# Kernel optimization log

Measured on AMD Instinct MI355X. Metric: run time of the kernel, lower is better.

## Reference

```python
import jax, jax.numpy as jnp
import numpy as np

B, D, I, H, K = 1024, 128, 64, 256, 8
HE = 2 * H  # encoder cell width (mu || log_sigma2)


def setup_inputs() -> dict:
    key = jax.random.key(0)
    ks = jax.random.split(key, 20)
    g = lambda i, shape, s=0.05: jax.random.normal(ks[i], shape, dtype=jnp.float32) * s
    return dict(
        X=g(0, (B, D, I), 1.0),
        W=jax.random.randint(ks[1], (B, D, I), 0, 2).astype(jnp.int32),
        noise=g(2, (B, H), 1.0),
        A=g(3, (D, I)),  # imputation template (learned)
        enc_Wx=g(4, (I, 4 * HE)), enc_Wh=g(5, (HE, 4 * HE)), enc_b=jnp.zeros((4 * HE,), jnp.float32),
        enc_pi=g(6, (HE,)), enc_pf=g(7, (HE,)), enc_po=g(8, (HE,)),
        dec_Wx=g(9, (I, 4 * H)), dec_Wh=g(10, (H, 4 * H)), dec_b=jnp.zeros((4 * H,), jnp.float32),
        dec_pi=g(11, (H,)), dec_pf=g(12, (H,)), dec_po=g(13, (H,)),
        out_w=g(14, (H, I)), out_b=jnp.full((I,), 0.1, jnp.float32),
        mu_c_unscaled=g(15, (K, H)), sigma2_c_unscaled=g(16, (K, H)), phi_c_unscaled=g(17, (K,)),
    )


def peephole_lstm(x_seq, Wx, Wh, b, pi, pf, po, h0, c0):
    """Keras PeepholeLSTMCell, gate order i,f,c,o. x_seq: [T,B,I] -> (hs [T,B,n], hT, cT)."""
    def step(carry, x):
        h, c = carry
        z = x @ Wx + h @ Wh + b
        zi, zf, zc, zo = jnp.split(z, 4, axis=-1)
        i = jax.nn.sigmoid(zi + pi * c)
        f = jax.nn.sigmoid(zf + pf * c)
        c_new = f * c + i * jnp.tanh(zc)
        o = jax.nn.sigmoid(zo + po * c_new)
        h_new = o * jnp.tanh(c_new)
        return (h_new, c_new), h_new
    (hT, cT), hs = jax.lax.scan(step, (h0, c0), x_seq)
    return hs, hT, cT


def reference(X, W, noise, A, enc_Wx, enc_Wh, enc_b, enc_pi, enc_pf, enc_po,
              dec_Wx, dec_Wh, dec_b, dec_pi, dec_pf, dec_po,
              out_w, out_b, mu_c_unscaled, sigma2_c_unscaled, phi_c_unscaled):
    Bn = X.shape[0]
    Wf = W.astype(X.dtype)
    X_imp = X * Wf + A * (1.0 - Wf)  # masked imputation
    # --- encode: peephole LSTM, take FINAL CELL STATE (encoder_rnn(...)[-1]) ---
    x_seq = jnp.swapaxes(X_imp, 0, 1)  # [D,B,I]
    h0 = jnp.zeros((Bn, HE), X.dtype)
    _, _, cT = peephole_lstm(x_seq, enc_Wx, enc_Wh, enc_b, enc_pi, enc_pf, enc_po, h0, h0)
    mu_tilde = cT[:, :H]
    log_sigma2_tilde = cT[:, H:]
    z = mu_tilde + jnp.exp(0.5 * log_sigma2_tilde) * noise
    # --- decode: zero inputs, initial_state = (h=0, c=z) ---
    dec_in = jnp.zeros((D, Bn, I), X.dtype)
    hs, _, _ = peephole_lstm(dec_in, dec_Wx, dec_Wh, dec_b, dec_pi, dec_pf, dec_po,
                             jnp.zeros((Bn, H), X.dtype), z)
    rnn_out = jnp.swapaxes(hs, 0, 1)  # [B,D,H]
    x_raw = rnn_out @ out_w + out_b   # [B,D,I]
    x = jax.nn.sigmoid(x_raw)
    # --- GMM parameters ---
    mu_c = mu_c_unscaled
    sigma2_c = jax.nn.softplus(sigma2_c_unscaled)
    phi_c = jax.nn.softmax(phi_c_unscaled)
    return (x, x_raw, mu_c, sigma2_c, phi_c, z, mu_tilde, log_sigma2_tilde)
```

## Files before the change

kernel.cpp:

```cpp
#include <hip/hip_runtime.h>
#include <hip/hip_bf16.h>

typedef __attribute__((ext_vector_type(4))) float f32x4;
typedef __attribute__((ext_vector_type(8))) short bf16x8;

#define NB 1024
#define ND 128
#define NI 64
#define NH 256
#define NHE 512
#define KENC 576
#define NENC 2048
#define KDEC 256
#define ESTR 584
#define DSTR 264

__device__ __forceinline__ float sigmf(float x) { return 1.0f / (1.0f + __expf(-x)); }
__device__ __forceinline__ float tanh_f(float x) { return 1.0f - 2.0f / (__expf(2.0f * x) + 1.0f); }

__device__ __forceinline__ f32x4 mfma16(bf16x8 a, bf16x8 b, f32x4 c) {
    return __builtin_amdgcn_mfma_f32_16x16x32_bf16(a, b, c, 0, 0, 0);
}

__device__ __forceinline__ void st_ull(unsigned long long* p, unsigned long long v) {
    __hip_atomic_store(p, v, __ATOMIC_RELAXED, __HIP_MEMORY_SCOPE_AGENT);
}
__device__ __forceinline__ unsigned long long ld_ull(const unsigned long long* p) {
    return __hip_atomic_load(p, __ATOMIC_RELAXED, __HIP_MEMORY_SCOPE_AGENT);
}
__device__ __forceinline__ void st_flag(int* p) {
    __hip_atomic_store(p, 1, __ATOMIC_RELAXED, __HIP_MEMORY_SCOPE_AGENT);
}

__device__ __forceinline__ void wspin(const int* flags, int n, int lane, const int* extra) {
    int g = 0;
    for (;;) {
        int v = 1;
        if (lane < n)
            v = __hip_atomic_load(flags + lane, __ATOMIC_RELAXED, __HIP_MEMORY_SCOPE_AGENT);
        else if (extra != nullptr && lane == n)
            v = __hip_atomic_load(extra, __ATOMIC_RELAXED, __HIP_MEMORY_SCOPE_AGENT);
        if (__all(v != 0)) return;
        __builtin_amdgcn_s_sleep(1);
        if (++g > (1 << 20)) return;
    }
}

__device__ __forceinline__ void quadtr(f32x4 a, int lane,
                                       float& z0, float& z1, float& z2, float& z3) {
    float x0 = a[0], x1 = a[1], x2 = a[2], x3 = a[3];
    float s0 = __shfl_xor(x0, 1), s1 = __shfl_xor(x1, 1),
          s2 = __shfl_xor(x2, 1), s3 = __shfl_xor(x3, 1);
    bool o1 = (lane & 1) != 0;
    float y0 = o1 ? s1 : x0;
    float y1 = o1 ? x1 : s0;
    float y2 = o1 ? s3 : x2;
    float y3 = o1 ? x3 : s2;
    float t0 = __shfl_xor(y0, 2), t1 = __shfl_xor(y1, 2),
          t2 = __shfl_xor(y2, 2), t3 = __shfl_xor(y3, 2);
    bool o2 = (lane & 2) != 0;
    z0 = o2 ? t2 : y0;
    z1 = o2 ? t3 : y1;
    z2 = o2 ? y2 : t0;
    z3 = o2 ? y3 : t1;
}


__global__ void pack_enc_kernel(const float* __restrict__ Wx, const float* __restrict__ Wh,
                                const float* __restrict__ bsrc,
                                __hip_bfloat16* __restrict__ Wp, float* __restrict__ bp)
{
    int n = blockIdx.y;
    int k = blockIdx.x * 256 + threadIdx.x;
    int j = n >> 2, g = n & 3;
    int col = g * NHE + j;
    if (k < KENC) {
        float v = (k < NI) ? Wx[k * NENC + col] : Wh[(k - NI) * NENC + col];
        Wp[(size_t)n * KENC + k] = __float2bfloat16(v);
    }
    if (blockIdx.x == 0 && threadIdx.x == 0) bp[n] = bsrc[col];
}

__global__ void pack_dec_kernel(const float* __restrict__ Wh, const float* __restrict__ ow,
                                const float* __restrict__ bsrc,
                                __hip_bfloat16* __restrict__ Wp, float* __restrict__ bp)
{
    int n = blockIdx.y;
    int k = threadIdx.x;
    float v;
    if (n < 1024) {
        int j = n >> 2, g = n & 3;
        int col = g * NH + j;
        v = Wh[k * 1024 + col];
        if (k == 0) bp[n] = bsrc[col];
    } else if (n < 1088) {
        v = ow[k * NI + (n - 1024)];
    } else {
        v = 0.0f;
    }
    Wp[(size_t)n * KDEC + k] = __float2bfloat16(v);
}

__global__ void pack_xb_kernel(const float* __restrict__ X, const int* __restrict__ W,
                               const float* __restrict__ A, __hip_bfloat16* __restrict__ Xb)
{
    int idx = blockIdx.x * 256 + threadIdx.x;
    int i = idx & 63;
    int t1 = idx >> 6;
    int b = t1 & 1023;
    int d = t1 >> 10;
    int src = (b * ND + d) * NI + i;
    float v = W[src] ? X[src] : A[d * NI + i];
    Xb[idx] = __float2bfloat16(v);
}

__global__ __launch_bounds__(256, 2) void enc_persist(
    const __hip_bfloat16* __restrict__ Xb,
    __hip_bfloat16* __restrict__ h0buf, __hip_bfloat16* __restrict__ h1buf,
    float* __restrict__ cenc,
    const __hip_bfloat16* __restrict__ Wp, const float* __restrict__ bp,
    const float* __restrict__ pi, const float* __restrict__ pf, const float* __restrict__ po,
    int* __restrict__ encfl)
{
    __shared__ __align__(16) unsigned short Alds[32][ESTR];
    __shared__ __align__(16) unsigned short Hlds[32][36];

    const int tid  = threadIdx.x;
    const int lane = tid & 63;
    const int wv   = tid >> 6;
    const int bm   = blockIdx.x;
    const int bn   = blockIdx.y;
    const int m0   = bm * 32;
    const int lr   = lane & 15;
    const int q    = lane >> 4;
    const int lk   = q * 8;

    bf16x8 breg[2][18];
    #pragma unroll
    for (int ni = 0; ni < 2; ++ni) {
        const __hip_bfloat16* wb = Wp + (size_t)(bn * 128 + wv * 32 + ni * 16 + lr) * KENC + lk;
        #pragma unroll
        for (int i = 0; i < 18; ++i)
            breg[ni][i] = *reinterpret_cast<const bf16x8*>(wb + i * 32);
    }

    const int u = lr >> 2;
    const int e = lane & 3;
    float4 bb[2];
    float ppi[2], ppf[2], ppo[2];
    int jl[2];
    #pragma unroll
    for (int ni = 0; ni < 2; ++ni) {
        jl[ni] = wv * 8 + ni * 4 + u;
        int jg = bn * 32 + jl[ni];
        bb[ni] = *reinterpret_cast<const float4*>(bp + 4 * jg);
        ppi[ni] = pi[jg]; ppf[ni] = pf[jg]; ppo[ni] = po[jg];
    }
    const int rowb = 4 * q + e;

    float creg[2][2] = {{0.f, 0.f}, {0.f, 0.f}};
    __hip_bfloat16* hbuf[2] = {h0buf, h1buf};

    for (int t = 0; t < ND; ++t) {
        {
            int row = tid >> 3, ch = tid & 7;
            *reinterpret_cast<bf16x8*>(&Alds[row][ch * 8]) =
                *reinterpret_cast<const bf16x8*>(Xb + ((size_t)t * NB + m0 + row) * NI + ch * 8);
        }
        __syncthreads();

        f32x4 acc[2][2];
        #pragma unroll
        for (int mi = 0; mi < 2; ++mi)
            #pragma unroll
            for (int ni = 0; ni < 2; ++ni) acc[mi][ni] = {0.f, 0.f, 0.f, 0.f};
        #pragma unroll
        for (int i = 0; i < 2; ++i) {
            bf16x8 a[2];
            #pragma unroll
            for (int mi = 0; mi < 2; ++mi)
                a[mi] = *reinterpret_cast<const bf16x8*>(&Alds[16 * mi + lr][i * 32 + lk]);
            #pragma unroll
            for (int mi = 0; mi < 2; ++mi)
                #pragma unroll
                for (int ni = 0; ni < 2; ++ni)
                    acc[mi][ni] = mfma16(a[mi], breg[ni][i], acc[mi][ni]);
        }

        if (t > 0) wspin(encfl + (size_t)(bm * ND + (t - 1)) * 16, 16, lane, nullptr);

        {
            const unsigned long long* hsrc =
                (const unsigned long long*)(hbuf[t & 1] + (size_t)m0 * NHE);
            #pragma unroll
            for (int it = 0; it < 16; ++it) {
                int idx = tid + it * 256;
                int row = idx >> 7, c8 = idx & 127;
                unsigned long long v = ld_ull(hsrc + (size_t)row * 128 + c8);
                *reinterpret_cast<unsigned long long*>(&Alds[row][64 + c8 * 4]) = v;
            }
        }
        __syncthreads();

        #pragma unroll
        for (int i = 2; i < 18; ++i) {
            bf16x8 a[2];
            #pragma unroll
            for (int mi = 0; mi < 2; ++mi)
                a[mi] = *reinterpret_cast<const bf16x8*>(&Alds[16 * mi + lr][i * 32 + lk]);
            #pragma unroll
            for (int mi = 0; mi < 2; ++mi)
                #pragma unroll
                for (int ni = 0; ni < 2; ++ni)
                    acc[mi][ni] = mfma16(a[mi], breg[ni][i], acc[mi][ni]);
        }

        #pragma unroll
        for (int mi = 0; mi < 2; ++mi) {
            #pragma unroll
            for (int ni = 0; ni < 2; ++ni) {
                float z0, z1, z2, z3;
                quadtr(acc[mi][ni], lane, z0, z1, z2, z3);
                float c_old = creg[mi][ni];
                float gi = sigmf(z0 + bb[ni].x + ppi[ni] * c_old);
                float gf = sigmf(z1 + bb[ni].y + ppf[ni] * c_old);
                float cn = gf * c_old + gi * tanh_f(z2 + bb[ni].z);
                float go = sigmf(z3 + bb[ni].w + ppo[ni] * cn);
                creg[mi][ni] = cn;
                int row = 16 * mi + rowb;
                __hip_bfloat16 hv = __float2bfloat16(go * tanh_f(cn));
                Hlds[row][jl[ni]] = reinterpret_cast<unsigned short&>(hv);
                if (t == ND - 1)
                    cenc[(size_t)(m0 + row) * NHE + bn * 32 + jl[ni]] = cn;
            }
        }
        __syncthreads();

        if (t < ND - 1) {
            {
                int row = tid >> 3, k8 = tid & 7;
                __hip_bfloat16* hdst = hbuf[(t + 1) & 1];
                unsigned long long v =
                    *reinterpret_cast<const unsigned long long*>(&Hlds[row][k8 * 4]);
                st_ull((unsigned long long*)(hdst + (size_t)(m0 + row) * NHE + bn * 32 + k8 * 4), v);
            }
            __syncthreads();
            if (tid == 0) st_flag(encfl + (size_t)(bm * ND + t) * 16 + bn);
        }
    }
}

__global__ __launch_bounds__(256, 2) void dec_persist(
    __hip_bfloat16* __restrict__ hd0, __hip_bfloat16* __restrict__ hd1,
    const float* __restrict__ zdec,
    const __hip_bfloat16* __restrict__ Wp, const float* __restrict__ bp,
    const float* __restrict__ pi, const float* __restrict__ pf, const float* __restrict__ po,
    const float* __restrict__ ob,
    float* __restrict__ ox, float* __restrict__ oxr,
    int* __restrict__ decfl, int* __restrict__ decpr)
{
    __shared__ __align__(16) unsigned short Alds[32][DSTR];
    __shared__ __align__(16) unsigned short Hlds[32][36];

    const int tid  = threadIdx.x;
    const int lane = tid & 63;
    const int wv   = tid >> 6;
    const int bm   = blockIdx.x;
    const int bn   = blockIdx.y;
    const int m0   = bm * 32;
    const int lr   = lane & 15;
    const int q    = lane >> 4;
    const int lk   = q * 8;

    __hip_bfloat16* hbuf[2] = {hd0, hd1};

    if (bn < 8) {
        bf16x8 breg[2][8];
        #pragma unroll
        for (int ni = 0; ni < 2; ++ni) {
            const __hip_bfloat16* wb = Wp + (size_t)(bn * 128 + wv * 32 + ni * 16 + lr) * KDEC + lk;
            #pragma unroll
            for (int i = 0; i < 8; ++i)
                breg[ni][i] = *reinterpret_cast<const bf16x8*>(wb + i * 32);
        }

        const int u = lr >> 2;
        const int e = lane & 3;
        float4 bb[2];
        float ppi[2], ppf[2], ppo[2];
        int jl[2];
        #pragma unroll
        for (int ni = 0; ni < 2; ++ni) {
            jl[ni] = wv * 8 + ni * 4 + u;
            int jg = bn * 32 + jl[ni];
            bb[ni] = *reinterpret_cast<const float4*>(bp + 4 * jg);
            ppi[ni] = pi[jg]; ppf[ni] = pf[jg]; ppo[ni] = po[jg];
        }
        const int rowb = 4 * q + e;

        float creg[2][2];
        #pragma unroll
        for (int mi = 0; mi < 2; ++mi)
            #pragma unroll
            for (int ni = 0; ni < 2; ++ni)
                creg[mi][ni] = zdec[(size_t)(m0 + 16 * mi + rowb) * NH + bn * 32 + jl[ni]];

        for (int t = 0; t < ND; ++t) {
            if (t >= 1) {
                const int* ex = (t >= 2) ? (decpr + bm * ND + (t - 2)) : nullptr;
                wspin(decfl + (size_t)(bm * ND + (t - 1)) * 8, 8, lane, ex);
            }

            {
                const unsigned long long* hsrc =
                    (const unsigned long long*)(hbuf[t & 1] + (size_t)m0 * NH);
                #pragma unroll
                for (int it = 0; it < 8; ++it) {
                    int idx = tid + it * 256;
                    int row = idx >> 6, c8 = idx & 63;
                    unsigned long long v = ld_ull(hsrc + (size_t)row * 64 + c8);
                    *reinterpret_cast<unsigned long long*>(&Alds[row][c8 * 4]) = v;
                }
            }
            __syncthreads();

            f32x4 acc[2][2];
            #pragma unroll
            for (int mi = 0; mi < 2; ++mi)
                #pragma unroll
                for (int ni = 0; ni < 2; ++ni) acc[mi][ni] = {0.f, 0.f, 0.f, 0.f};
            #pragma unroll
            for (int i = 0; i < 8; ++i) {
                bf16x8 a[2];
                #pragma unroll
                for (int mi = 0; mi < 2; ++mi)
                    a[mi] = *reinterpret_cast<const bf16x8*>(&Alds[16 * mi + lr][i * 32 + lk]);
                #pragma unroll
                for (int mi = 0; mi < 2; ++mi)
                    #pragma unroll
                    for (int ni = 0; ni < 2; ++ni)
                        acc[mi][ni] = mfma16(a[mi], breg[ni][i], acc[mi][ni]);
            }

            #pragma unroll
            for (int mi = 0; mi < 2; ++mi) {
                #pragma unroll
                for (int ni = 0; ni < 2; ++ni) {
                    float z0, z1, z2, z3;
                    quadtr(acc[mi][ni], lane, z0, z1, z2, z3);
                    float c_old = creg[mi][ni];
                    float gi = sigmf(z0 + bb[ni].x + ppi[ni] * c_old);
                    float gf = sigmf(z1 + bb[ni].y + ppf[ni] * c_old);
                    float cn = gf * c_old + gi * tanh_f(z2 + bb[ni].z);
                    float go = sigmf(z3 + bb[ni].w + ppo[ni] * cn);
                    creg[mi][ni] = cn;
                    int row = 16 * mi + rowb;
                    __hip_bfloat16 hv = __float2bfloat16(go * tanh_f(cn));
                    Hlds[row][jl[ni]] = reinterpret_cast<unsigned short&>(hv);
                }
            }
            __syncthreads();

            {
                int row = tid >> 3, k8 = tid & 7;
                __hip_bfloat16* hdst = hbuf[(t + 1) & 1];
                unsigned long long v =
                    *reinterpret_cast<const unsigned long long*>(&Hlds[row][k8 * 4]);
                st_ull((unsigned long long*)(hdst + (size_t)(m0 + row) * NH + bn * 32 + k8 * 4), v);
            }
            __syncthreads();
            if (tid == 0) st_flag(decfl + (size_t)(bm * ND + t) * 8 + bn);
        }
    } else {
        bf16x8 breg[8];
        const __hip_bfloat16* wb = Wp + (size_t)(1024 + wv * 16 + lr) * KDEC + lk;
        #pragma unroll
        for (int i = 0; i < 8; ++i)
            breg[i] = *reinterpret_cast<const bf16x8*>(wb + i * 32);
        const float obv = ob[wv * 16 + lr];

        for (int s = 0; s < ND; ++s) {
            wspin(decfl + (size_t)(bm * ND + s) * 8, 8, lane, nullptr);
            __syncthreads();

            {
                const unsigned long long* hsrc =
                    (const unsigned long long*)(hbuf[(s + 1) & 1] + (size_t)m0 * NH);
                #pragma unroll
                for (int it = 0; it < 8; ++it) {
                    int idx = tid + it * 256;
                    int row = idx >> 6, c8 = idx & 63;
                    unsigned long long v = ld_ull(hsrc + (size_t)row * 64 + c8);
                    *reinterpret_cast<unsigned long long*>(&Alds[row][c8 * 4]) = v;
                }
            }
            __syncthreads();
            if (tid == 0) st_flag(decpr + bm * ND + s);

            f32x4 acc[2];
            #pragma unroll
            for (int mi = 0; mi < 2; ++mi) acc[mi] = {0.f, 0.f, 0.f, 0.f};
            #pragma unroll
            for (int i = 0; i < 8; ++i) {
                bf16x8 a[2];
                #pragma unroll
                for (int mi = 0; mi < 2; ++mi)
                    a[mi] = *reinterpret_cast<const bf16x8*>(&Alds[16 * mi + lr][i * 32 + lk]);
                #pragma unroll
                for (int mi = 0; mi < 2; ++mi)
                    acc[mi] = mfma16(a[mi], breg[i], acc[mi]);
            }

            int colp = wv * 16 + lr;
            #pragma unroll
            for (int mi = 0; mi < 2; ++mi) {
                #pragma unroll
                for (int v = 0; v < 4; ++v) {
                    int row = m0 + 16 * mi + 4 * q + v;
                    float val = acc[mi][v] + obv;
                    size_t off = (size_t)row * (ND * NI) + (size_t)s * NI + colp;
                    oxr[off] = val;
                    ox[off]  = sigmf(val);
                }
            }
        }
    }
}

__global__ void mid_kernel(const float* __restrict__ cenc, const float* __restrict__ noise,
                           float* __restrict__ zdec, float* __restrict__ oz,
                           float* __restrict__ omut, float* __restrict__ olst)
{
    int idx = blockIdx.x * 256 + threadIdx.x;
    int b = idx >> 8, h = idx & 255;
    float mu = cenc[b * NHE + h];
    float ls = cenc[b * NHE + NH + h];
    float zz = mu + expf(0.5f * ls) * noise[idx];
    omut[idx] = mu;
    olst[idx] = ls;
    oz[idx]   = zz;
    zdec[idx] = zz;
}

__global__ void mix_kernel(const float* __restrict__ mu_in, const float* __restrict__ s2_in,
                           const float* __restrict__ phi_in,
                           float* __restrict__ mu_out, float* __restrict__ s2_out,
                           float* __restrict__ phi_out)
{
    int idx = blockIdx.x * 256 + threadIdx.x;
    mu_out[idx] = mu_in[idx];
    float x = s2_in[idx];
    s2_out[idx] = (x > 20.0f) ? x : log1pf(expf(x));
    if (idx == 0) {
        float m = phi_in[0];
        for (int k = 1; k < 8; ++k) m = fmaxf(m, phi_in[k]);
        float e[8], s = 0.0f;
        for (int k = 0; k < 8; ++k) { e[k] = expf(phi_in[k] - m); s += e[k]; }
        for (int k = 0; k < 8; ++k) phi_out[k] = e[k] / s;
    }
}

extern "C" void kernel_launch(void* const* d_in, const int* in_sizes, int n_in,
                              void* d_out, int out_size, void* d_ws, size_t ws_size,
                              hipStream_t stream)
{
    const float* X     = (const float*)d_in[0];
    const int*   W     = (const int*)d_in[1];
    const float* noise = (const float*)d_in[2];
    const float* A     = (const float*)d_in[3];
    const float* eWx   = (const float*)d_in[4];
    const float* eWh   = (const float*)d_in[5];
    const float* eb    = (const float*)d_in[6];
    const float* epi   = (const float*)d_in[7];
    const float* epf   = (const float*)d_in[8];
    const float* epo   = (const float*)d_in[9];
    const float* dWh   = (const float*)d_in[11];
    const float* db    = (const float*)d_in[12];
    const float* dpi   = (const float*)d_in[13];
    const float* dpf   = (const float*)d_in[14];
    const float* dpo   = (const float*)d_in[15];
    const float* ow    = (const float*)d_in[16];
    const float* ob    = (const float*)d_in[17];
    const float* muc   = (const float*)d_in[18];
    const float* s2c   = (const float*)d_in[19];
    const float* phic  = (const float*)d_in[20];

    float* out = (float*)d_out;
    float* o_x    = out;
    float* o_xraw = out + 8388608;
    float* o_muc  = out + 16777216;
    float* o_s2c  = out + 16779264;
    float* o_phic = out + 16781312;
    float* o_z    = out + 16781320;
    float* o_mut  = out + 17043464;
    float* o_lst  = out + 17305608;

    char* ws = (char*)d_ws;
    __hip_bfloat16* Wencp = (__hip_bfloat16*)(ws + 0);
    __hip_bfloat16* Wdecp = (__hip_bfloat16*)(ws + 2359296);
    float*          bencp = (float*)(ws + 2949120);
    float*          bdecp = (float*)(ws + 2957312);
    __hip_bfloat16* Xb    = (__hip_bfloat16*)(ws + 2965504);
    __hip_bfloat16* he0   = (__hip_bfloat16*)(ws + 19742720);
    __hip_bfloat16* he1   = (__hip_bfloat16*)(ws + 20791296);
    float*          cenc  = (float*)(ws + 21839872);
    __hip_bfloat16* hd0   = (__hip_bfloat16*)(ws + 23937024);
    __hip_bfloat16* hd1   = (__hip_bfloat16*)(ws + 24461312);
    float*          zdec  = (float*)(ws + 24985600);
    int*            encfl = (int*)(ws + 26034176);
    int*            decfl = (int*)(ws + 26296320);
    int*            decpr = (int*)(ws + 26427392);

    hipMemsetAsync(he0, 0, 1048576, stream);
    hipMemsetAsync(hd0, 0, 524288, stream);
    hipMemsetAsync(encfl, 0, 409600, stream);

    pack_enc_kernel<<<dim3(3, 2048), 256, 0, stream>>>(eWx, eWh, eb, Wencp, bencp);
    pack_dec_kernel<<<dim3(1, 1152), 256, 0, stream>>>(dWh, ow, db, Wdecp, bdecp);
    pack_xb_kernel<<<32768, 256, 0, stream>>>(X, W, A, Xb);

    enc_persist<<<dim3(32, 16), 256, 0, stream>>>(
        Xb, he0, he1, cenc, Wencp, bencp, epi, epf, epo, encfl);

    mid_kernel<<<1024, 256, 0, stream>>>(cenc, noise, zdec, o_z, o_mut, o_lst);
    mix_kernel<<<8, 256, 0, stream>>>(muc, s2c, phic, o_muc, o_s2c, o_phic);

    dec_persist<<<dim3(32, 9), 256, 0, stream>>>(
        hd0, hd1, zdec, Wdecp, bdecp, dpi, dpf, dpo, ob, o_x, o_xraw, decfl, decpr);
}
```

Before: 1.703 ms.

## Replace encoder flag barriers with step-tagged hidden-state words

The encoder's inter-block handoff drops separate per-step flags. Each 64-bit word now carries three bf16 hidden values plus a 16-bit step tag, and consumers poll the data words directly until the tag matches. This removes the flag store, the extra syncthreads and the flag spin from the per-step critical path. In exchange, the hidden buffer grows, packing and unpacking costs more, the x-input MFMAs no longer overlap with the wait, and correctness relies on each 64-bit atomic store landing as a single unit.

```diff
diff --git a/kernel.cpp b/kernel.cpp
--- a/kernel.cpp
+++ b/kernel.cpp
@@ -14,6 +14,7 @@
 #define KDEC 256
 #define ESTR 584
 #define DSTR 264
+#define HWPR 176
 
 __device__ __forceinline__ float sigmf(float x) { return 1.0f / (1.0f + __expf(-x)); }
 __device__ __forceinline__ float tanh_f(float x) { return 1.0f - 2.0f / (__expf(2.0f * x) + 1.0f); }
@@ -116,11 +117,10 @@
 
 __global__ __launch_bounds__(256, 2) void enc_persist(
     const __hip_bfloat16* __restrict__ Xb,
-    __hip_bfloat16* __restrict__ h0buf, __hip_bfloat16* __restrict__ h1buf,
+    unsigned long long* __restrict__ hw0, unsigned long long* __restrict__ hw1,
     float* __restrict__ cenc,
     const __hip_bfloat16* __restrict__ Wp, const float* __restrict__ bp,
-    const float* __restrict__ pi, const float* __restrict__ pf, const float* __restrict__ po,
-    int* __restrict__ encfl)
+    const float* __restrict__ pi, const float* __restrict__ pf, const float* __restrict__ po)
 {
     __shared__ __align__(16) unsigned short Alds[32][ESTR];
     __shared__ __align__(16) unsigned short Hlds[32][36];
@@ -159,7 +159,7 @@
     const int rowb = 4 * q + e;
 
     float creg[2][2] = {{0.f, 0.f}, {0.f, 0.f}};
-    __hip_bfloat16* hbuf[2] = {h0buf, h1buf};
+    unsigned long long* hwb[2] = {hw0, hw1};
 
     for (int t = 0; t < ND; ++t) {
         {
@@ -167,6 +167,57 @@
             *reinterpret_cast<bf16x8*>(&Alds[row][ch * 8]) =
                 *reinterpret_cast<const bf16x8*>(Xb + ((size_t)t * NB + m0 + row) * NI + ch * 8);
         }
+
+        {
+            const unsigned long long* hsrc = hwb[t & 1] + (size_t)m0 * HWPR;
+            unsigned long long v[22];
+            #pragma unroll
+            for (int it = 0; it < 22; ++it)
+                v[it] = ld_ull(hsrc + tid + it * 256);
+
+            bool bad[22];
+            bool anybad = false;
+            #pragma unroll
+            for (int it = 0; it < 22; ++it) {
+                bool ok = ((int)(v[it] >> 48) == t);
+                bad[it] = !ok;
+                anybad |= !ok;
+                if (ok) {
+                    int idx = tid + it * 256;
+                    int row = idx / HWPR, rem = idx - row * HWPR;
+                    int p = rem / 11, w = rem - p * 11;
+                    int c0 = 64 + p * 32 + 3 * w;
+                    #pragma unroll
+                    for (int j = 0; j < 3; ++j)
+                        if (3 * w + j < 32)
+                            Alds[row][c0 + j] = (unsigned short)(v[it] >> (16 * j));
+                }
+            }
+            int g = 0;
+            while (anybad && ++g < (1 << 20)) {
+                anybad = false;
+                #pragma unroll
+                for (int it = 0; it < 22; ++it) {
+                    if (bad[it]) {
+                        unsigned long long x = ld_ull(hsrc + tid + it * 256);
+                        if ((int)(x >> 48) == t) {
+                            int idx = tid + it * 256;
+                            int row = idx / HWPR, rem = idx - row * HWPR;
+                            int p = rem / 11, w = rem - p * 11;
+                            int c0 = 64 + p * 32 + 3 * w;
+                            #pragma unroll
+                            for (int j = 0; j < 3; ++j)
+                                if (3 * w + j < 32)
+                                    Alds[row][c0 + j] = (unsigned short)(x >> (16 * j));
+                            bad[it] = false;
+                        } else {
+                            anybad = true;
+                        }
+                    }
+                }
+                if (anybad) __builtin_amdgcn_s_sleep(1);
+            }
+        }
         __syncthreads();
 
         f32x4 acc[2][2];
@@ -175,35 +226,7 @@
             #pragma unroll
             for (int ni = 0; ni < 2; ++ni) acc[mi][ni] = {0.f, 0.f, 0.f, 0.f};
         #pragma unroll
-        for (int i = 0; i < 2; ++i) {
-            bf16x8 a[2];
-            #pragma unroll
-            for (int mi = 0; mi < 2; ++mi)
-                a[mi] = *reinterpret_cast<const bf16x8*>(&Alds[16 * mi + lr][i * 32 + lk]);
-            #pragma unroll
-            for (int mi = 0; mi < 2; ++mi)
-                #pragma unroll
-                for (int ni = 0; ni < 2; ++ni)
-                    acc[mi][ni] = mfma16(a[mi], breg[ni][i], acc[mi][ni]);
-        }
-
-        if (t > 0) wspin(encfl + (size_t)(bm * ND + (t - 1)) * 16, 16, lane, nullptr);
-
-        {
-            const unsigned long long* hsrc =
-                (const unsigned long long*)(hbuf[t & 1] + (size_t)m0 * NHE);
-            #pragma unroll
-            for (int it = 0; it < 16; ++it) {
-                int idx = tid + it * 256;
-                int row = idx >> 7, c8 = idx & 127;
-                unsigned long long v = ld_ull(hsrc + (size_t)row * 128 + c8);
-                *reinterpret_cast<unsigned long long*>(&Alds[row][64 + c8 * 4]) = v;
-            }
-        }
-        __syncthreads();
-
-        #pragma unroll
-        for (int i = 2; i < 18; ++i) {
+        for (int i = 0; i < 18; ++i) {
             bf16x8 a[2];
             #pragma unroll
             for (int mi = 0; mi < 2; ++mi)
@@ -237,16 +260,19 @@
         __syncthreads();
 
         if (t < ND - 1) {
-            {
-                int row = tid >> 3, k8 = tid & 7;
-                __hip_bfloat16* hdst = hbuf[(t + 1) & 1];
-                unsigned long long v =
-                    *reinterpret_cast<const unsigned long long*>(&Hlds[row][k8 * 4]);
-                st_ull((unsigned long long*)(hdst + (size_t)(m0 + row) * NHE + bn * 32 + k8 * 4), v);
-            }
-            __syncthreads();
-            if (tid == 0) st_flag(encfl + (size_t)(bm * ND + t) * 16 + bn);
-        }
+            unsigned long long* hdst = hwb[(t + 1) & 1] + (size_t)m0 * HWPR + bn * 11;
+            const unsigned long long tag = (unsigned long long)(unsigned)(t + 1) << 48;
+            for (int idx = tid; idx < 352; idx += 256) {
+                int row = idx / 11, w = idx - row * 11;
+                unsigned long long v = tag;
+                #pragma unroll
+                for (int j = 0; j < 3; ++j)
+                    if (3 * w + j < 32)
+                        v |= (unsigned long long)Hlds[row][3 * w + j] << (16 * j);
+                st_ull(hdst + (size_t)row * HWPR + w, v);
+            }
+        }
+        __syncthreads();
     }
 }
 
@@ -501,26 +527,25 @@
     float*          bencp = (float*)(ws + 2949120);
     float*          bdecp = (float*)(ws + 2957312);
     __hip_bfloat16* Xb    = (__hip_bfloat16*)(ws + 2965504);
-    __hip_bfloat16* he0   = (__hip_bfloat16*)(ws + 19742720);
-    __hip_bfloat16* he1   = (__hip_bfloat16*)(ws + 20791296);
-    float*          cenc  = (float*)(ws + 21839872);
-    __hip_bfloat16* hd0   = (__hip_bfloat16*)(ws + 23937024);
-    __hip_bfloat16* hd1   = (__hip_bfloat16*)(ws + 24461312);
-    float*          zdec  = (float*)(ws + 24985600);
-    int*            encfl = (int*)(ws + 26034176);
-    int*            decfl = (int*)(ws + 26296320);
-    int*            decpr = (int*)(ws + 26427392);
-
-    hipMemsetAsync(he0, 0, 1048576, stream);
+    unsigned long long* hw0 = (unsigned long long*)(ws + 19742720);
+    unsigned long long* hw1 = (unsigned long long*)(ws + 21184512);
+    float*          cenc  = (float*)(ws + 22626304);
+    __hip_bfloat16* hd0   = (__hip_bfloat16*)(ws + 24723456);
+    __hip_bfloat16* hd1   = (__hip_bfloat16*)(ws + 25247744);
+    float*          zdec  = (float*)(ws + 25772032);
+    int*            decfl = (int*)(ws + 26820608);
+    int*            decpr = (int*)(ws + 26951680);
+
+    hipMemsetAsync(hw0, 0, 2883584, stream);
     hipMemsetAsync(hd0, 0, 524288, stream);
-    hipMemsetAsync(encfl, 0, 409600, stream);
+    hipMemsetAsync(decfl, 0, 147456, stream);
 
     pack_enc_kernel<<<dim3(3, 2048), 256, 0, stream>>>(eWx, eWh, eb, Wencp, bencp);
     pack_dec_kernel<<<dim3(1, 1152), 256, 0, stream>>>(dWh, ow, db, Wdecp, bdecp);
     pack_xb_kernel<<<32768, 256, 0, stream>>>(X, W, A, Xb);
 
     enc_persist<<<dim3(32, 16), 256, 0, stream>>>(
-        Xb, he0, he1, cenc, Wencp, bencp, epi, epf, epo, encfl);
+        Xb, hw0, hw1, cenc, Wencp, bencp, epi, epf, epo);
 
     mid_kernel<<<1024, 256, 0, stream>>>(cenc, noise, zdec, o_z, o_mut, o_lst);
     mix_kernel<<<8, 256, 0, stream>>>(muc, s2c, phic, o_muc, o_s2c, o_phic);
```

Measured after the change: 3.923 ms. +130.3%, slower.

## Halve row tile in persistent LSTM kernels and signal readiness per wave

Applied to the files above, without the earlier changes.

Both persistent recurrent kernels now handle 16 batch rows per block instead of 32, which doubles the grid and raises launch bounds to 4 blocks per CU. The goal is more concurrent waves to hide per-step latency. The trailing block barrier before the ready flag is replaced by a vmcnt wait and one flag per wave, and consumers spin on four times as many flags. The h stores become 32-bit. In exchange, the encoder weights held in registers (36 bf16x8 per lane) may not fit under the tighter register budget and could spill. The persistent spin-wait scheme also now depends on 1024 encoder blocks being co-resident at once.

```diff
diff --git a/kernel.cpp b/kernel.cpp
--- a/kernel.cpp
+++ b/kernel.cpp
@@ -22,7 +22,7 @@
     return __builtin_amdgcn_mfma_f32_16x16x32_bf16(a, b, c, 0, 0, 0);
 }
 
-__device__ __forceinline__ void st_ull(unsigned long long* p, unsigned long long v) {
+__device__ __forceinline__ void st_u32(unsigned* p, unsigned v) {
     __hip_atomic_store(p, v, __ATOMIC_RELAXED, __HIP_MEMORY_SCOPE_AGENT);
 }
 __device__ __forceinline__ unsigned long long ld_ull(const unsigned long long* p) {
@@ -114,7 +114,7 @@
     Xb[idx] = __float2bfloat16(v);
 }
 
-__global__ __launch_bounds__(256, 2) void enc_persist(
+__global__ __launch_bounds__(256, 4) void enc_persist(
     const __hip_bfloat16* __restrict__ Xb,
     __hip_bfloat16* __restrict__ h0buf, __hip_bfloat16* __restrict__ h1buf,
     float* __restrict__ cenc,
@@ -122,15 +122,15 @@
     const float* __restrict__ pi, const float* __restrict__ pf, const float* __restrict__ po,
     int* __restrict__ encfl)
 {
-    __shared__ __align__(16) unsigned short Alds[32][ESTR];
-    __shared__ __align__(16) unsigned short Hlds[32][36];
+    __shared__ __align__(16) unsigned short Alds[16][ESTR];
+    __shared__ __align__(16) unsigned short Hlds[16][36];
 
     const int tid  = threadIdx.x;
     const int lane = tid & 63;
     const int wv   = tid >> 6;
     const int bm   = blockIdx.x;
     const int bn   = blockIdx.y;
-    const int m0   = bm * 32;
+    const int m0   = bm * 16;
     const int lr   = lane & 15;
     const int q    = lane >> 4;
     const int lk   = q * 8;
@@ -158,42 +158,35 @@
     }
     const int rowb = 4 * q + e;
 
-    float creg[2][2] = {{0.f, 0.f}, {0.f, 0.f}};
+    float creg[2] = {0.f, 0.f};
     __hip_bfloat16* hbuf[2] = {h0buf, h1buf};
 
     for (int t = 0; t < ND; ++t) {
-        {
+        if (tid < 128) {
             int row = tid >> 3, ch = tid & 7;
             *reinterpret_cast<bf16x8*>(&Alds[row][ch * 8]) =
                 *reinterpret_cast<const bf16x8*>(Xb + ((size_t)t * NB + m0 + row) * NI + ch * 8);
         }
         __syncthreads();
 
-        f32x4 acc[2][2];
-        #pragma unroll
-        for (int mi = 0; mi < 2; ++mi)
-            #pragma unroll
-            for (int ni = 0; ni < 2; ++ni) acc[mi][ni] = {0.f, 0.f, 0.f, 0.f};
+        f32x4 acc[2];
+        #pragma unroll
+        for (int ni = 0; ni < 2; ++ni) acc[ni] = {0.f, 0.f, 0.f, 0.f};
         #pragma unroll
         for (int i = 0; i < 2; ++i) {
-            bf16x8 a[2];
-            #pragma unroll
-            for (int mi = 0; mi < 2; ++mi)
-                a[mi] = *reinterpret_cast<const bf16x8*>(&Alds[16 * mi + lr][i * 32 + lk]);
-            #pragma unroll
-            for (int mi = 0; mi < 2; ++mi)
-                #pragma unroll
-                for (int ni = 0; ni < 2; ++ni)
-                    acc[mi][ni] = mfma16(a[mi], breg[ni][i], acc[mi][ni]);
-        }
-
-        if (t > 0) wspin(encfl + (size_t)(bm * ND + (t - 1)) * 16, 16, lane, nullptr);
+            bf16x8 a = *reinterpret_cast<const bf16x8*>(&Alds[lr][i * 32 + lk]);
+            #pragma unroll
+            for (int ni = 0; ni < 2; ++ni)
+                acc[ni] = mfma16(a, breg[ni][i], acc[ni]);
+        }
+
+        if (t > 0) wspin(encfl + (size_t)(bm * ND + (t - 1)) * 64, 64, lane, nullptr);
 
         {
             const unsigned long long* hsrc =
                 (const unsigned long long*)(hbuf[t & 1] + (size_t)m0 * NHE);
             #pragma unroll
-            for (int it = 0; it < 16; ++it) {
+            for (int it = 0; it < 8; ++it) {
                 int idx = tid + it * 256;
                 int row = idx >> 7, c8 = idx & 127;
                 unsigned long long v = ld_ull(hsrc + (size_t)row * 128 + c8);
@@ -204,53 +197,44 @@
 
         #pragma unroll
         for (int i = 2; i < 18; ++i) {
-            bf16x8 a[2];
-            #pragma unroll
-            for (int mi = 0; mi < 2; ++mi)
-                a[mi] = *reinterpret_cast<const bf16x8*>(&Alds[16 * mi + lr][i * 32 + lk]);
-            #pragma unroll
-            for (int mi = 0; mi < 2; ++mi)
-                #pragma unroll
-                for (int ni = 0; ni < 2; ++ni)
-                    acc[mi][ni] = mfma16(a[mi], breg[ni][i], acc[mi][ni]);
-        }
-
-        #pragma unroll
-        for (int mi = 0; mi < 2; ++mi) {
-            #pragma unroll
-            for (int ni = 0; ni < 2; ++ni) {
-                float z0, z1, z2, z3;
-                quadtr(acc[mi][ni], lane, z0, z1, z2, z3);
-                float c_old = creg[mi][ni];
-                float gi = sigmf(z0 + bb[ni].x + ppi[ni] * c_old);
-                float gf = sigmf(z1 + bb[ni].y + ppf[ni] * c_old);
-                float cn = gf * c_old + gi * tanh_f(z2 + bb[ni].z);
-                float go = sigmf(z3 + bb[ni].w + ppo[ni] * cn);
-                creg[mi][ni] = cn;
-                int row = 16 * mi + rowb;
-                __hip_bfloat16 hv = __float2bfloat16(go * tanh_f(cn));
-                Hlds[row][jl[ni]] = reinterpret_cast<unsigned short&>(hv);
-                if (t == ND - 1)
-                    cenc[(size_t)(m0 + row) * NHE + bn * 32 + jl[ni]] = cn;
-            }
+            bf16x8 a = *reinterpret_cast<const bf16x8*>(&Alds[lr][i * 32 + lk]);
+            #pragma unroll
+            for (int ni = 0; ni < 2; ++ni)
+                acc[ni] = mfma16(a, breg[ni][i], acc[ni]);
+        }
+
+        #pragma unroll
+        for (int ni = 0; ni < 2; ++ni) {
+            float z0, z1, z2, z3;
+            quadtr(acc[ni], lane, z0, z1, z2, z3);
+            float c_old = creg[ni];
+            float gi = sigmf(z0 + bb[ni].x + ppi[ni] * c_old);
+            float gf = sigmf(z1 + bb[ni].y + ppf[ni] * c_old);
+            float cn = gf * c_old + gi * tanh_f(z2 + bb[ni].z);
+            float go = sigmf(z3 + bb[ni].w + ppo[ni] * cn);
+            creg[ni] = cn;
+            __hip_bfloat16 hv = __float2bfloat16(go * tanh_f(cn));
+            Hlds[rowb][jl[ni]] = reinterpret_cast<unsigned short&>(hv);
+            if (t == ND - 1)
+                cenc[(size_t)(m0 + rowb) * NHE + bn * 32 + jl[ni]] = cn;
         }
         __syncthreads();
 
         if (t < ND - 1) {
             {
-                int row = tid >> 3, k8 = tid & 7;
+                int row = tid >> 4, k4 = tid & 15;
                 __hip_bfloat16* hdst = hbuf[(t + 1) & 1];
-                unsigned long long v =
-                    *reinterpret_cast<const unsigned long long*>(&Hlds[row][k8 * 4]);
-                st_ull((unsigned long long*)(hdst + (size_t)(m0 + row) * NHE + bn * 32 + k8 * 4), v);
-            }
-            __syncthreads();
-            if (tid == 0) st_flag(encfl + (size_t)(bm * ND + t) * 16 + bn);
-        }
-    }
-}
-
-__global__ __launch_bounds__(256, 2) void dec_persist(
+                unsigned v = *reinterpret_cast<const unsigned*>(&Hlds[row][k4 * 2]);
+                st_u32(reinterpret_cast<unsigned*>(hdst + (size_t)(m0 + row) * NHE + bn * 32) + k4, v);
+            }
+            asm volatile("s_waitcnt vmcnt(0)" ::: "memory");
+            if (lane == 0)
+                st_flag(encfl + (size_t)(bm * ND + t) * 64 + bn * 4 + wv);
+        }
+    }
+}
+
+__global__ __launch_bounds__(256, 4) void dec_persist(
     __hip_bfloat16* __restrict__ hd0, __hip_bfloat16* __restrict__ hd1,
     const float* __restrict__ zdec,
     const __hip_bfloat16* __restrict__ Wp, const float* __restrict__ bp,
@@ -259,15 +243,15 @@
     float* __restrict__ ox, float* __restrict__ oxr,
     int* __restrict__ decfl, int* __restrict__ decpr)
 {
-    __shared__ __align__(16) unsigned short Alds[32][DSTR];
-    __shared__ __align__(16) unsigned short Hlds[32][36];
+    __shared__ __align__(16) unsigned short Alds[16][DSTR];
+    __shared__ __align__(16) unsigned short Hlds[16][36];
 
     const int tid  = threadIdx.x;
     const int lane = tid & 63;
     const int wv   = tid >> 6;
     const int bm   = blockIdx.x;
     const int bn   = blockIdx.y;
-    const int m0   = bm * 32;
+    const int m0   = bm * 16;
     const int lr   = lane & 15;
     const int q    = lane >> 4;
     const int lk   = q * 8;
@@ -298,24 +282,22 @@
         }
         const int rowb = 4 * q + e;
 
-        float creg[2][2];
-        #pragma unroll
-        for (int mi = 0; mi < 2; ++mi)
-            #pragma unroll
-            for (int ni = 0; ni < 2; ++ni)
-                creg[mi][ni] = zdec[(size_t)(m0 + 16 * mi + rowb) * NH + bn * 32 + jl[ni]];
+        float creg[2];
+        #pragma unroll
+        for (int ni = 0; ni < 2; ++ni)
+            creg[ni] = zdec[(size_t)(m0 + rowb) * NH + bn * 32 + jl[ni]];
 
         for (int t = 0; t < ND; ++t) {
             if (t >= 1) {
                 const int* ex = (t >= 2) ? (decpr + bm * ND + (t - 2)) : nullptr;
-                wspin(decfl + (size_t)(bm * ND + (t - 1)) * 8, 8, lane, ex);
+                wspin(decfl + (size_t)(bm * ND + (t - 1)) * 32, 32, lane, ex);
             }
 
             {
                 const unsigned long long* hsrc =
                     (const unsigned long long*)(hbuf[t & 1] + (size_t)m0 * NH);
                 #pragma unroll
-                for (int it = 0; it < 8; ++it) {
+                for (int it = 0; it < 4; ++it) {
                     int idx = tid + it * 256;
                     int row = idx >> 6, c8 = idx & 63;
                     unsigned long long v = ld_ull(hsrc + (size_t)row * 64 + c8);
@@ -324,52 +306,41 @@
             }
             __syncthreads();
 
-            f32x4 acc[2][2];
-            #pragma unroll
-            for (int mi = 0; mi < 2; ++mi)
+            f32x4 acc[2];
+            #pragma unroll
+            for (int ni = 0; ni < 2; ++ni) acc[ni] = {0.f, 0.f, 0.f, 0.f};
+            #pragma unroll
+            for (int i = 0; i < 8; ++i) {
+                bf16x8 a = *reinterpret_cast<const bf16x8*>(&Alds[lr][i * 32 + lk]);
                 #pragma unroll
-                for (int ni = 0; ni < 2; ++ni) acc[mi][ni] = {0.f, 0.f, 0.f, 0.f};
-            #pragma unroll
-            for (int i = 0; i < 8; ++i) {
-                bf16x8 a[2];
-                #pragma unroll
-                for (int mi = 0; mi < 2; ++mi)
-                    a[mi] = *reinterpret_cast<const bf16x8*>(&Alds[16 * mi + lr][i * 32 + lk]);
-                #pragma unroll
-                for (int mi = 0; mi < 2; ++mi)
-                    #pragma unroll
-                    for (int ni = 0; ni < 2; ++ni)
-                        acc[mi][ni] = mfma16(a[mi], breg[ni][i], acc[mi][ni]);
-            }
-
-            #pragma unroll
-            for (int mi = 0; mi < 2; ++mi) {
-                #pragma unroll
-                for (int ni = 0; ni < 2; ++ni) {
-                    float z0, z1, z2, z3;
-                    quadtr(acc[mi][ni], lane, z0, z1, z2, z3);
-                    float c_old = creg[mi][ni];
-                    float gi = sigmf(z0 + bb[ni].x + ppi[ni] * c_old);
-                    float gf = sigmf(z1 + bb[ni].y + ppf[ni] * c_old);
-                    float cn = gf * c_old + gi * tanh_f(z2 + bb[ni].z);
-                    float go = sigmf(z3 + bb[ni].w + ppo[ni] * cn);
-                    creg[mi][ni] = cn;
-                    int row = 16 * mi + rowb;
-                    __hip_bfloat16 hv = __float2bfloat16(go * tanh_f(cn));
-                    Hlds[row][jl[ni]] = reinterpret_cast<unsigned short&>(hv);
-                }
+                for (int ni = 0; ni < 2; ++ni)
+                    acc[ni] = mfma16(a, breg[ni][i], acc[ni]);
+            }
+
+            #pragma unroll
+            for (int ni = 0; ni < 2; ++ni) {
+                float z0, z1, z2, z3;
+                quadtr(acc[ni], lane, z0, z1, z2, z3);
+                float c_old = creg[ni];
+                float gi = sigmf(z0 + bb[ni].x + ppi[ni] * c_old);
+                float gf = sigmf(z1 + bb[ni].y + ppf[ni] * c_old);
+                float cn = gf * c_old + gi * tanh_f(z2 + bb[ni].z);
+                float go = sigmf(z3 + bb[ni].w + ppo[ni] * cn);
+                creg[ni] = cn;
+                __hip_bfloat16 hv = __float2bfloat16(go * tanh_f(cn));
+                Hlds[rowb][jl[ni]] = reinterpret_cast<unsigned short&>(hv);
             }
             __syncthreads();
 
             {
-                int row = tid >> 3, k8 = tid & 7;
+                int row = tid >> 4, k4 = tid & 15;
                 __hip_bfloat16* hdst = hbuf[(t + 1) & 1];
-                unsigned long long v =
-                    *reinterpret_cast<const unsigned long long*>(&Hlds[row][k8 * 4]);
-                st_ull((unsigned long long*)(hdst + (size_t)(m0 + row) * NH + bn * 32 + k8 * 4), v);
-            }
-            __syncthreads();
-            if (tid == 0) st_flag(decfl + (size_t)(bm * ND + t) * 8 + bn);
+                unsigned v = *reinterpret_cast<const unsigned*>(&Hlds[row][k4 * 2]);
+                st_u32(reinterpret_cast<unsigned*>(hdst + (size_t)(m0 + row) * NH + bn * 32) + k4, v);
+            }
+            asm volatile("s_waitcnt vmcnt(0)" ::: "memory");
+            if (lane == 0)
+                st_flag(decfl + (size_t)(bm * ND + t) * 32 + bn * 4 + wv);
         }
     } else {
         bf16x8 breg[8];
@@ -380,14 +351,14 @@
         const float obv = ob[wv * 16 + lr];
 
         for (int s = 0; s < ND; ++s) {
-            wspin(decfl + (size_t)(bm * ND + s) * 8, 8, lane, nullptr);
+            wspin(decfl + (size_t)(bm * ND + s) * 32, 32, lane, nullptr);
             __syncthreads();
 
             {
                 const unsigned long long* hsrc =
                     (const unsigned long long*)(hbuf[(s + 1) & 1] + (size_t)m0 * NH);
                 #pragma unroll
-                for (int it = 0; it < 8; ++it) {
+                for (int it = 0; it < 4; ++it) {
                     int idx = tid + it * 256;
                     int row = idx >> 6, c8 = idx & 63;
                     unsigned long long v = ld_ull(hsrc + (size_t)row * 64 + c8);
@@ -397,31 +368,21 @@
             __syncthreads();
             if (tid == 0) st_flag(decpr + bm * ND + s);
 
-            f32x4 acc[2];
-            #pragma unroll
-            for (int mi = 0; mi < 2; ++mi) acc[mi] = {0.f, 0.f, 0.f, 0.f};
+            f32x4 acc = {0.f, 0.f, 0.f, 0.f};
             #pragma unroll
             for (int i = 0; i < 8; ++i) {
-                bf16x8 a[2];
-                #pragma unroll
-                for (int mi = 0; mi < 2; ++mi)
-                    a[mi] = *reinterpret_cast<const bf16x8*>(&Alds[16 * mi + lr][i * 32 + lk]);
-                #pragma unroll
-                for (int mi = 0; mi < 2; ++mi)
-                    acc[mi] = mfma16(a[mi], breg[i], acc[mi]);
+                bf16x8 a = *reinterpret_cast<const bf16x8*>(&Alds[lr][i * 32 + lk]);
+                acc = mfma16(a, breg[i], acc);
             }
 
             int colp = wv * 16 + lr;
             #pragma unroll
-            for (int mi = 0; mi < 2; ++mi) {
-                #pragma unroll
-                for (int v = 0; v < 4; ++v) {
-                    int row = m0 + 16 * mi + 4 * q + v;
-                    float val = acc[mi][v] + obv;
-                    size_t off = (size_t)row * (ND * NI) + (size_t)s * NI + colp;
-                    oxr[off] = val;
-                    ox[off]  = sigmf(val);
-                }
+            for (int v = 0; v < 4; ++v) {
+                int row = m0 + 4 * q + v;
+                float val = acc[v] + obv;
+                size_t off = (size_t)row * (ND * NI) + (size_t)s * NI + colp;
+                oxr[off] = val;
+                ox[off]  = sigmf(val);
             }
         }
     }
@@ -508,23 +469,23 @@
     __hip_bfloat16* hd1   = (__hip_bfloat16*)(ws + 24461312);
     float*          zdec  = (float*)(ws + 24985600);
     int*            encfl = (int*)(ws + 26034176);
-    int*            decfl = (int*)(ws + 26296320);
-    int*            decpr = (int*)(ws + 26427392);
+    int*            decfl = (int*)(ws + 28131328);
+    int*            decpr = (int*)(ws + 29179904);
 
     hipMemsetAsync(he0, 0, 1048576, stream);
     hipMemsetAsync(hd0, 0, 524288, stream);
-    hipMemsetAsync(encfl, 0, 409600, stream);
+    hipMemsetAsync(encfl, 0, 3178496, stream);
 
     pack_enc_kernel<<<dim3(3, 2048), 256, 0, stream>>>(eWx, eWh, eb, Wencp, bencp);
     pack_dec_kernel<<<dim3(1, 1152), 256, 0, stream>>>(dWh, ow, db, Wdecp, bdecp);
     pack_xb_kernel<<<32768, 256, 0, stream>>>(X, W, A, Xb);
 
-    enc_persist<<<dim3(32, 16), 256, 0, stream>>>(
+    enc_persist<<<dim3(64, 16), 256, 0, stream>>>(
         Xb, he0, he1, cenc, Wencp, bencp, epi, epf, epo, encfl);
 
     mid_kernel<<<1024, 256, 0, stream>>>(cenc, noise, zdec, o_z, o_mut, o_lst);
     mix_kernel<<<8, 256, 0, stream>>>(muc, s2c, phic, o_muc, o_s2c, o_phic);
 
-    dec_persist<<<dim3(32, 9), 256, 0, stream>>>(
+    dec_persist<<<dim3(64, 9), 256, 0, stream>>>(
         hd0, hd1, zdec, Wdecp, bdecp, dpi, dpf, dpo, ob, o_x, o_xraw, decfl, decpr);
 }
```

After: 2.832 ms. +66.3%, slower.

## Use per-wave completion flags instead of block barrier before flag publish

Applied to the files above, without the earlier changes.

Each wave now drains its own global stores and sets a per-wave flag, replacing the block-wide __syncthreads plus a single thread flag. Consumers spin on 4x more flags (64 for the encoder, 32 for the decoder) through the lanes of one wave. The encoder also stops running the X-input MFMAs before the spin and does all 18 k-steps after the h load, and the h load indexing is simplified to linear addressing. This removes a barrier from the recurrent critical path, at the cost of more flag traffic, a larger flag memset, and losing the overlap of the input GEMM with the wait.

```diff
diff --git a/kernel.cpp b/kernel.cpp
--- a/kernel.cpp
+++ b/kernel.cpp
@@ -30,6 +30,9 @@
 }
 __device__ __forceinline__ void st_flag(int* p) {
     __hip_atomic_store(p, 1, __ATOMIC_RELAXED, __HIP_MEMORY_SCOPE_AGENT);
+}
+__device__ __forceinline__ void drain_vm() {
+    asm volatile("s_waitcnt vmcnt(0)" ::: "memory");
 }
 
 __device__ __forceinline__ void wspin(const int* flags, int n, int lane, const int* extra) {
@@ -167,27 +170,8 @@
             *reinterpret_cast<bf16x8*>(&Alds[row][ch * 8]) =
                 *reinterpret_cast<const bf16x8*>(Xb + ((size_t)t * NB + m0 + row) * NI + ch * 8);
         }
-        __syncthreads();
-
-        f32x4 acc[2][2];
-        #pragma unroll
-        for (int mi = 0; mi < 2; ++mi)
-            #pragma unroll
-            for (int ni = 0; ni < 2; ++ni) acc[mi][ni] = {0.f, 0.f, 0.f, 0.f};
-        #pragma unroll
-        for (int i = 0; i < 2; ++i) {
-            bf16x8 a[2];
-            #pragma unroll
-            for (int mi = 0; mi < 2; ++mi)
-                a[mi] = *reinterpret_cast<const bf16x8*>(&Alds[16 * mi + lr][i * 32 + lk]);
-            #pragma unroll
-            for (int mi = 0; mi < 2; ++mi)
-                #pragma unroll
-                for (int ni = 0; ni < 2; ++ni)
-                    acc[mi][ni] = mfma16(a[mi], breg[ni][i], acc[mi][ni]);
-        }
-
-        if (t > 0) wspin(encfl + (size_t)(bm * ND + (t - 1)) * 16, 16, lane, nullptr);
+
+        if (t > 0) wspin(encfl + (size_t)(bm * ND + (t - 1)) * 64, 64, lane, nullptr);
 
         {
             const unsigned long long* hsrc =
@@ -195,15 +179,20 @@
             #pragma unroll
             for (int it = 0; it < 16; ++it) {
                 int idx = tid + it * 256;
-                int row = idx >> 7, c8 = idx & 127;
-                unsigned long long v = ld_ull(hsrc + (size_t)row * 128 + c8);
-                *reinterpret_cast<unsigned long long*>(&Alds[row][64 + c8 * 4]) = v;
+                unsigned long long v = ld_ull(hsrc + idx);
+                *reinterpret_cast<unsigned long long*>(
+                    &Alds[idx >> 7][64 + (idx & 127) * 4]) = v;
             }
         }
         __syncthreads();
 
-        #pragma unroll
-        for (int i = 2; i < 18; ++i) {
+        f32x4 acc[2][2];
+        #pragma unroll
+        for (int mi = 0; mi < 2; ++mi)
+            #pragma unroll
+            for (int ni = 0; ni < 2; ++ni) acc[mi][ni] = {0.f, 0.f, 0.f, 0.f};
+        #pragma unroll
+        for (int i = 0; i < 18; ++i) {
             bf16x8 a[2];
             #pragma unroll
             for (int mi = 0; mi < 2; ++mi)
@@ -244,8 +233,9 @@
                     *reinterpret_cast<const unsigned long long*>(&Hlds[row][k8 * 4]);
                 st_ull((unsigned long long*)(hdst + (size_t)(m0 + row) * NHE + bn * 32 + k8 * 4), v);
             }
-            __syncthreads();
-            if (tid == 0) st_flag(encfl + (size_t)(bm * ND + t) * 16 + bn);
+            drain_vm();
+            if (lane == 0)
+                st_flag(encfl + (size_t)(bm * ND + t) * 64 + bn * 4 + wv);
         }
     }
 }
@@ -308,7 +298,7 @@
         for (int t = 0; t < ND; ++t) {
             if (t >= 1) {
                 const int* ex = (t >= 2) ? (decpr + bm * ND + (t - 2)) : nullptr;
-                wspin(decfl + (size_t)(bm * ND + (t - 1)) * 8, 8, lane, ex);
+                wspin(decfl + (size_t)(bm * ND + (t - 1)) * 32, 32, lane, ex);
             }
 
             {
@@ -317,9 +307,9 @@
                 #pragma unroll
                 for (int it = 0; it < 8; ++it) {
                     int idx = tid + it * 256;
-                    int row = idx >> 6, c8 = idx & 63;
-                    unsigned long long v = ld_ull(hsrc + (size_t)row * 64 + c8);
-                    *reinterpret_cast<unsigned long long*>(&Alds[row][c8 * 4]) = v;
+                    unsigned long long v = ld_ull(hsrc + idx);
+                    *reinterpret_cast<unsigned long long*>(
+                        &Alds[idx >> 6][(idx & 63) * 4]) = v;
                 }
             }
             __syncthreads();
@@ -368,8 +358,9 @@
                     *reinterpret_cast<const unsigned long long*>(&Hlds[row][k8 * 4]);
                 st_ull((unsigned long long*)(hdst + (size_t)(m0 + row) * NH + bn * 32 + k8 * 4), v);
             }
-            __syncthreads();
-            if (tid == 0) st_flag(decfl + (size_t)(bm * ND + t) * 8 + bn);
+            drain_vm();
+            if (lane == 0)
+                st_flag(decfl + (size_t)(bm * ND + t) * 32 + bn * 4 + wv);
         }
     } else {
         bf16x8 breg[8];
@@ -380,7 +371,7 @@
         const float obv = ob[wv * 16 + lr];
 
         for (int s = 0; s < ND; ++s) {
-            wspin(decfl + (size_t)(bm * ND + s) * 8, 8, lane, nullptr);
+            wspin(decfl + (size_t)(bm * ND + s) * 32, 32, lane, nullptr);
             __syncthreads();
 
             {
@@ -389,9 +380,9 @@
                 #pragma unroll
                 for (int it = 0; it < 8; ++it) {
                     int idx = tid + it * 256;
-                    int row = idx >> 6, c8 = idx & 63;
-                    unsigned long long v = ld_ull(hsrc + (size_t)row * 64 + c8);
-                    *reinterpret_cast<unsigned long long*>(&Alds[row][c8 * 4]) = v;
+                    unsigned long long v = ld_ull(hsrc + idx);
+                    *reinterpret_cast<unsigned long long*>(
+                        &Alds[idx >> 6][(idx & 63) * 4]) = v;
                 }
             }
             __syncthreads();
@@ -508,12 +499,12 @@
     __hip_bfloat16* hd1   = (__hip_bfloat16*)(ws + 24461312);
     float*          zdec  = (float*)(ws + 24985600);
     int*            encfl = (int*)(ws + 26034176);
-    int*            decfl = (int*)(ws + 26296320);
-    int*            decpr = (int*)(ws + 26427392);
+    int*            decfl = (int*)(ws + 27082752);
+    int*            decpr = (int*)(ws + 27607040);
 
     hipMemsetAsync(he0, 0, 1048576, stream);
     hipMemsetAsync(hd0, 0, 524288, stream);
-    hipMemsetAsync(encfl, 0, 409600, stream);
+    hipMemsetAsync(encfl, 0, 1589248, stream);
 
     pack_enc_kernel<<<dim3(3, 2048), 256, 0, stream>>>(eWx, eWh, eb, Wencp, bencp);
     pack_dec_kernel<<<dim3(1, 1152), 256, 0, stream>>>(dWh, ow, db, Wdecp, bdecp);
```

Measured after the change: 2.111 ms. +24.0%, slower.
